# Optimization experiments

Measured on AMD Instinct MI355X. Metric: run time of the kernel, lower is better.

## Reference

```python
import jax, jax.numpy as jnp
import numpy as np

B, F, D, H = 16384, 10, 512, 8
DH = D // H
EPS = 1e-5


def setup_inputs() -> dict:
    key = jax.random.key(0)
    ks = jax.random.split(key, 12)
    s = 1.0 / np.sqrt(D)
    inp = {
        "x": jax.random.normal(ks[0], (B, F), dtype=jnp.float32),
        # per-feature Linear(1, D): weight (F, D), bias (F, D)
        "Wf": jax.random.normal(ks[1], (F, D), dtype=jnp.float32) * 1.0,
        "bf": jax.random.normal(ks[2], (F, D), dtype=jnp.float32) * 0.1,
        # MHA in/out projections (torch layout: out_features x in_features)
        "Wq": jax.random.normal(ks[3], (D, D), dtype=jnp.float32) * s,
        "Wk": jax.random.normal(ks[4], (D, D), dtype=jnp.float32) * s,
        "Wv": jax.random.normal(ks[5], (D, D), dtype=jnp.float32) * s,
        "bq": jax.random.normal(ks[6], (D,), dtype=jnp.float32) * 0.02,
        "bk": jax.random.normal(ks[7], (D,), dtype=jnp.float32) * 0.02,
        "bv": jax.random.normal(ks[8], (D,), dtype=jnp.float32) * 0.02,
        "Wo": jax.random.normal(ks[9], (D, D), dtype=jnp.float32) * s,
        "bo": jax.random.normal(ks[10], (D,), dtype=jnp.float32) * 0.02,
        "gamma": jnp.ones((D,), dtype=jnp.float32),
        "beta": jnp.zeros((D,), dtype=jnp.float32),
    }
    return inp


def reference(x, Wf, bf, Wq, Wk, Wv, bq, bk, bv, Wo, bo, gamma, beta):
    # Fused per-feature scalar Linear + ReLU: (B,F,1)*(F,D) + (F,D) -> (B,F,D)
    p = jax.nn.relu(x[:, :, None] * Wf[None] + bf[None])
    # Multi-head self-attention (q = k = v = p), torch Linear: y = x @ W.T + b
    def heads(t):  # (B,F,D) -> (B,H,F,DH)
        return t.reshape(B, F, H, DH).transpose(0, 2, 1, 3)
    q = heads(p @ Wq.T + bq)
    k = heads(p @ Wk.T + bk)
    v = heads(p @ Wv.T + bv)
    scores = jnp.einsum("bhqd,bhkd->bhqk", q, k) / jnp.sqrt(jnp.float32(DH))
    attn = jax.nn.softmax(scores, axis=-1)
    o = jnp.einsum("bhqk,bhkd->bhqd", attn, v)
    o = o.transpose(0, 2, 1, 3).reshape(B, F, D) @ Wo.T + bo
    # LayerNorm over last dim
    mu = jnp.mean(o, axis=-1, keepdims=True)
    var = jnp.mean(jnp.square(o - mu), axis=-1, keepdims=True)
    ln = (o - mu) * jax.lax.rsqrt(var + EPS) * gamma + beta
    # sum pool over the function/sequence axis
    return jnp.sum(ln, axis=1)  # (B, D)
```

## Files before the change

### kernel.cpp

```cpp
#include <hip/hip_runtime.h>
#include <stdint.h>


typedef __bf16 bf16;
typedef __bf16 bf16x8 __attribute__((ext_vector_type(8)));
typedef float f32x4 __attribute__((ext_vector_type(4)));

#define EPS 1e-5f

static constexpr size_t O_ELEMS   = (size_t)16384 * 10 * 512;
static constexpr size_t O_BYTES   = O_ELEMS * 2;
static constexpr size_t WQKV_ELEMS = (size_t)8 * 192 * 512;
static constexpr size_t WQKV_BYTES = WQKV_ELEMS * 2;

__device__ __forceinline__ void async_copy16(void* lds, const void* g) {
  __builtin_amdgcn_global_load_lds(
      (const __attribute__((address_space(1))) uint32_t*)g,
      (__attribute__((address_space(3))) uint32_t*)lds, 16, 0, 0);
}

__global__ __launch_bounds__(256) void pack_weights(
    const float* __restrict__ Wq, const float* __restrict__ Wk,
    const float* __restrict__ Wv, const float* __restrict__ Wo,
    bf16* __restrict__ wqkv, bf16* __restrict__ wob) {
  int idx = blockIdx.x * 256 + threadIdx.x;
#pragma unroll
  for (int u = 0; u < 4; ++u) {
    int i = idx + u * 262144;
    if (i < 786432) {
      int pr = i >> 9, k = i & 511;
      int h = pr / 192, w = pr - h * 192;
      int t = w >> 6, r = w & 63;
      const float* src = (t == 0) ? Wq : ((t == 1) ? Wk : Wv);
      wqkv[i] = (bf16)src[(h * 64 + r) * 512 + k];
    } else {
      int j = i - 786432;
      wob[j] = (bf16)Wo[j];
    }
  }
}

__global__ __launch_bounds__(256, 2) void kern_attn(
    const float* __restrict__ x, const float* __restrict__ Wf,
    const float* __restrict__ bfv, const bf16* __restrict__ wqkv,
    const float* __restrict__ bq, const float* __restrict__ bk,
    const float* __restrict__ bv, bf16* __restrict__ O) {
  __shared__ __align__(16) char sA[8 * 48 * 128];
  __shared__ __align__(16) char sU[24576];
  bf16* qkv = (bf16*)sU;
  float* sc = (float*)(sU + 19200);

  const int tid = threadIdx.x;
  const int wave = tid >> 6;
  const int lane = tid & 63;
  const int lm = lane & 15;
  const int lg = lane >> 4;
  const int b0 = blockIdx.x * 4;

#pragma unroll
  for (int it = 0; it < 12; ++it) {
    int c = tid + it * 256;
    int s = c / 384, rem = c - s * 384;
    int r = rem >> 3, kcp = rem & 7;
    int kc = kcp ^ (r & 7);
    int k = s * 64 + kc * 8;
    bf16x8 pv;
    if (r < 40) {
      int bl = r / 10, f = r - bl * 10;
      float xv = x[(b0 + bl) * 10 + f];
      const float* wf = Wf + f * 512 + k;
      const float* bp = bfv + f * 512 + k;
#pragma unroll
      for (int j = 0; j < 8; ++j) {
        float p = fmaxf(xv * wf[j] + bp[j], 0.f);
        pv[j] = (bf16)p;
      }
    } else {
#pragma unroll
      for (int j = 0; j < 8; ++j) pv[j] = (bf16)0.f;
    }
    *(bf16x8*)(sA + s * 6144 + r * 128 + kcp * 16) = pv;
  }

  const int lr = lane >> 3;
  const int kcp2 = lane & 7;
  const int kcg = kcp2 ^ lr;

  for (int h = 0; h < 8; ++h) {
    f32x4 acc[3][3];
#pragma unroll
    for (int i = 0; i < 3; ++i)
#pragma unroll
      for (int j = 0; j < 3; ++j) { f32x4 z = {0.f, 0.f, 0.f, 0.f}; acc[i][j] = z; }

    const bf16* wh = wqkv + (size_t)h * 192 * 512;

    for (int s = 0; s < 8; ++s) {
#pragma unroll
      for (int jb = 0; jb < 6; ++jb) {
        int rb = wave + 4 * jb;
        int rr = rb * 8 + lr;
        async_copy16(sU + rb * 1024, wh + (size_t)rr * 512 + s * 64 + kcg * 8);
      }
      __syncthreads();
#pragma unroll
      for (int kk = 0; kk < 2; ++kk) {
        int kcl = kk * 4 + lg;
        bf16x8 af[3], bfr[3];
#pragma unroll
        for (int mt = 0; mt < 3; ++mt) {
          int m = mt * 16 + lm;
          af[mt] = *(const bf16x8*)(sA + s * 6144 + m * 128 + ((kcl ^ (m & 7)) << 4));
        }
#pragma unroll
        for (int nt = 0; nt < 3; ++nt) {
          int n = wave * 48 + nt * 16 + lm;
          bfr[nt] = *(const bf16x8*)(sU + n * 128 + ((kcl ^ (n & 7)) << 4));
        }
#pragma unroll
        for (int mt = 0; mt < 3; ++mt)
#pragma unroll
          for (int nt = 0; nt < 3; ++nt)
            acc[mt][nt] = __builtin_amdgcn_mfma_f32_16x16x32_bf16(af[mt], bfr[nt], acc[mt][nt], 0, 0, 0);
      }
      __syncthreads();
    }

#pragma unroll
    for (int nt = 0; nt < 3; ++nt) {
      int col = wave * 48 + nt * 16 + lm;
      float bias;
      if (col < 64) bias = bq[h * 64 + col];
      else if (col < 128) bias = bk[h * 64 + col - 64];
      else bias = bv[h * 64 + col - 128];
#pragma unroll
      for (int mt = 0; mt < 3; ++mt)
#pragma unroll
        for (int r = 0; r < 4; ++r) {
          int row = mt * 16 + lg * 4 + r;
          if (row < 40) qkv[row * 200 + col] = (bf16)(acc[mt][nt][r] + bias);
        }
    }
    __syncthreads();

    {
      int b = wave;
#pragma unroll
      for (int pp = 0; pp < 2; ++pp) {
        int p = lane + pp * 64;
        if (p < 100) {
          int i = p / 10, j = p - i * 10;
          const bf16x8* qr = (const bf16x8*)(qkv + (b * 10 + i) * 200);
          const bf16x8* kr = (const bf16x8*)(qkv + (b * 10 + j) * 200 + 64);
          float d = 0.f;
#pragma unroll
          for (int c8 = 0; c8 < 8; ++c8) {
            bf16x8 qv = qr[c8], kv = kr[c8];
#pragma unroll
            for (int e = 0; e < 8; ++e) d += (float)qv[e] * (float)kv[e];
          }
          sc[(b * 10 + i) * 12 + j] = d * 0.125f;
        }
      }
    }
    __syncthreads();

    if (tid < 40) {
      float* row = sc + tid * 12;
      float m = row[0];
#pragma unroll
      for (int j = 1; j < 10; ++j) m = fmaxf(m, row[j]);
      float e[10], sum = 0.f;
#pragma unroll
      for (int j = 0; j < 10; ++j) { e[j] = __expf(row[j] - m); sum += e[j]; }
      float inv = 1.f / sum;
#pragma unroll
      for (int j = 0; j < 10; ++j) row[j] = e[j] * inv;
    }
    __syncthreads();

#pragma unroll
    for (int u = 0; u < 10; ++u) {
      int id = tid + u * 256;
      int b = id / 640, rem2 = id - b * 640;
      int i = rem2 >> 6, d = rem2 & 63;
      const float* ar = sc + (b * 10 + i) * 12;
      float o = 0.f;
#pragma unroll
      for (int j = 0; j < 10; ++j)
        o += ar[j] * (float)qkv[(b * 10 + j) * 200 + 128 + d];
      O[((size_t)(b0 + b) * 10 + i) * 512 + h * 64 + d] = (bf16)o;
    }
    __syncthreads();
  }
}

__global__ __launch_bounds__(256, 2) void kern_out(
    const bf16* __restrict__ O, const bf16* __restrict__ wob,
    const float* __restrict__ bo, const float* __restrict__ gamma,
    const float* __restrict__ beta, float* __restrict__ out) {
  __shared__ __align__(16) char sAB[71680];
  __shared__ float partial[48][4][2];
  __shared__ float stats[48][2];
  char* As = sAB;
  char* Bs = sAB + 6144;
  bf16* lnb = (bf16*)sAB;

  const int tid = threadIdx.x;
  const int wave = tid >> 6, lane = tid & 63;
  const int lm = lane & 15, lg = lane >> 4;
  const int m0 = blockIdx.x * 40;

  f32x4 acc[3][8];
#pragma unroll
  for (int i = 0; i < 3; ++i)
#pragma unroll
    for (int j = 0; j < 8; ++j) { f32x4 z = {0.f, 0.f, 0.f, 0.f}; acc[i][j] = z; }

  const int lr = lane >> 3;
  const int kcp2 = lane & 7;
  const int kcg = kcp2 ^ lr;

  for (int s = 0; s < 8; ++s) {
    {
      int rr = wave * 8 + lr;
      int rm = min(rr, 39);
      async_copy16(As + wave * 1024, O + (size_t)(m0 + rm) * 512 + s * 64 + kcg * 8);
      if (wave < 2) {
        int rr2 = (4 + wave) * 8 + lr;
        int rm2 = min(rr2, 39);
        async_copy16(As + (4 + wave) * 1024, O + (size_t)(m0 + rm2) * 512 + s * 64 + kcg * 8);
      }
    }
#pragma unroll
    for (int jb = 0; jb < 16; ++jb) {
      int rb = wave + 4 * jb;
      int n = rb * 8 + lr;
      async_copy16(Bs + rb * 1024, wob + (size_t)n * 512 + s * 64 + kcg * 8);
    }
    __syncthreads();
#pragma unroll
    for (int kk = 0; kk < 2; ++kk) {
      int kcl = kk * 4 + lg;
      bf16x8 af[3], bfr[8];
#pragma unroll
      for (int mt = 0; mt < 3; ++mt) {
        int m = mt * 16 + lm;
        af[mt] = *(const bf16x8*)(As + m * 128 + ((kcl ^ (m & 7)) << 4));
      }
#pragma unroll
      for (int nt = 0; nt < 8; ++nt) {
        int n = wave * 128 + nt * 16 + lm;
        bfr[nt] = *(const bf16x8*)(Bs + n * 128 + ((kcl ^ (n & 7)) << 4));
      }
#pragma unroll
      for (int mt = 0; mt < 3; ++mt)
#pragma unroll
        for (int nt = 0; nt < 8; ++nt)
          acc[mt][nt] = __builtin_amdgcn_mfma_f32_16x16x32_bf16(af[mt], bfr[nt], acc[mt][nt], 0, 0, 0);
    }
    __syncthreads();
  }

#pragma unroll
  for (int nt = 0; nt < 8; ++nt) {
    int col = wave * 128 + nt * 16 + lm;
    float bb = bo[col];
#pragma unroll
    for (int mt = 0; mt < 3; ++mt)
#pragma unroll
      for (int r = 0; r < 4; ++r) acc[mt][nt][r] += bb;
  }

#pragma unroll
  for (int mt = 0; mt < 3; ++mt)
#pragma unroll
    for (int r = 0; r < 4; ++r) {
      float s1 = 0.f, s2 = 0.f;
#pragma unroll
      for (int nt = 0; nt < 8; ++nt) { float v = acc[mt][nt][r]; s1 += v; s2 += v * v; }
#pragma unroll
      for (int off = 1; off < 16; off <<= 1) {
        s1 += __shfl_xor(s1, off);
        s2 += __shfl_xor(s2, off);
      }
      if (lm == 0) {
        int row = mt * 16 + lg * 4 + r;
        partial[row][wave][0] = s1;
        partial[row][wave][1] = s2;
      }
    }
  __syncthreads();
  if (tid < 48) {
    float s1 = partial[tid][0][0] + partial[tid][1][0] + partial[tid][2][0] + partial[tid][3][0];
    float s2 = partial[tid][0][1] + partial[tid][1][1] + partial[tid][2][1] + partial[tid][3][1];
    float mu = s1 * (1.f / 512.f);
    float var = s2 * (1.f / 512.f) - mu * mu;
    stats[tid][0] = mu;
    stats[tid][1] = rsqrtf(var + EPS);
  }
  __syncthreads();
#pragma unroll
  for (int mt = 0; mt < 3; ++mt)
#pragma unroll
    for (int r = 0; r < 4; ++r) {
      int row = mt * 16 + lg * 4 + r;
      float mu = stats[row][0], rr = stats[row][1];
#pragma unroll
      for (int nt = 0; nt < 8; ++nt) {
        int col = wave * 128 + nt * 16 + lm;
        lnb[row * 520 + col] = (bf16)((acc[mt][nt][r] - mu) * rr);
      }
    }
  __syncthreads();
#pragma unroll
  for (int u = 0; u < 8; ++u) {
    int id = tid + u * 256;
    int b = id >> 9, n = id & 511;
    float ssum = 0.f;
#pragma unroll
    for (int f = 0; f < 10; ++f) ssum += (float)lnb[(b * 10 + f) * 520 + n];
    out[(size_t)(blockIdx.x * 4 + b) * 512 + n] = gamma[n] * ssum + 10.f * beta[n];
  }
}

extern "C" void kernel_launch(void* const* d_in, const int* in_sizes, int n_in,
                              void* d_out, int out_size, void* d_ws, size_t ws_size,
                              hipStream_t stream) {
  const float* x     = (const float*)d_in[0];
  const float* Wf    = (const float*)d_in[1];
  const float* bfv   = (const float*)d_in[2];
  const float* Wq    = (const float*)d_in[3];
  const float* Wk    = (const float*)d_in[4];
  const float* Wv    = (const float*)d_in[5];
  const float* bq    = (const float*)d_in[6];
  const float* bk    = (const float*)d_in[7];
  const float* bv    = (const float*)d_in[8];
  const float* Wo    = (const float*)d_in[9];
  const float* bo    = (const float*)d_in[10];
  const float* gamma = (const float*)d_in[11];
  const float* beta  = (const float*)d_in[12];
  float* out = (float*)d_out;

  char* ws = (char*)d_ws;
  bf16* O    = (bf16*)ws;
  bf16* wqkv = (bf16*)(ws + O_BYTES);
  bf16* wob  = (bf16*)(ws + O_BYTES + WQKV_BYTES);

  pack_weights<<<1024, 256, 0, stream>>>(Wq, Wk, Wv, Wo, wqkv, wob);
  kern_attn<<<4096, 256, 0, stream>>>(x, Wf, bfv, wqkv, bq, bk, bv, O);
  kern_out<<<4096, 256, 0, stream>>>(O, wob, bo, gamma, beta, out);
}
```

Measured before the change: 842.9 us.

## Give each wave its own heads with double-buffered weights and MFMA attention

The attention kernel now assigns whole heads to individual waves, two heads per wave, instead of splitting each head's QKV columns across the four waves. Each wave streams its head's weight slices into a private double-buffered LDS region using async loads and vmcnt waits, so block-wide barriers are gone from the main loop. Scores and the attention-times-V product are computed with MFMA over a block-diagonal 40x40 tile, with masked softmax done through shuffles and normalization deferred to the output. The trade-off is much more LDS per block and more registers (launch bounds drop to one block per CU), plus wasted MFMA work on the masked off-diagonal entries.

Result: slower. 910.1 us (+8.0%).

```diff
diff --git a/kernel.cpp b/kernel.cpp
--- a/kernel.cpp
+++ b/kernel.cpp
@@ -10,14 +10,15 @@
 
 static constexpr size_t O_ELEMS   = (size_t)16384 * 10 * 512;
 static constexpr size_t O_BYTES   = O_ELEMS * 2;
-static constexpr size_t WQKV_ELEMS = (size_t)8 * 192 * 512;
-static constexpr size_t WQKV_BYTES = WQKV_ELEMS * 2;
+static constexpr size_t WQKV_BYTES = (size_t)8 * 192 * 512 * 2;
 
 __device__ __forceinline__ void async_copy16(void* lds, const void* g) {
   __builtin_amdgcn_global_load_lds(
       (const __attribute__((address_space(1))) uint32_t*)g,
       (__attribute__((address_space(3))) uint32_t*)lds, 16, 0, 0);
 }
+__device__ __forceinline__ void wait_vmcnt_0()  { __builtin_amdgcn_s_waitcnt(0x0F70); }
+__device__ __forceinline__ void wait_vmcnt_12() { __builtin_amdgcn_s_waitcnt(0x0F70 | 12); }
 
 __global__ __launch_bounds__(256) void pack_weights(
     const float* __restrict__ Wq, const float* __restrict__ Wk,
@@ -40,15 +41,13 @@
   }
 }
 
-__global__ __launch_bounds__(256, 2) void kern_attn(
+__global__ __launch_bounds__(256, 1) void kern_attn(
     const float* __restrict__ x, const float* __restrict__ Wf,
     const float* __restrict__ bfv, const bf16* __restrict__ wqkv,
     const float* __restrict__ bq, const float* __restrict__ bk,
     const float* __restrict__ bv, bf16* __restrict__ O) {
-  __shared__ __align__(16) char sA[8 * 48 * 128];
-  __shared__ __align__(16) char sU[24576];
-  bf16* qkv = (bf16*)sU;
-  float* sc = (float*)(sU + 19200);
+  __shared__ __align__(16) char sA[49152];
+  __shared__ __align__(16) char sW[4][24576];
 
   const int tid = threadIdx.x;
   const int wave = tid >> 6;
@@ -71,127 +70,191 @@
       const float* wf = Wf + f * 512 + k;
       const float* bp = bfv + f * 512 + k;
 #pragma unroll
-      for (int j = 0; j < 8; ++j) {
-        float p = fmaxf(xv * wf[j] + bp[j], 0.f);
-        pv[j] = (bf16)p;
-      }
+      for (int j = 0; j < 8; ++j) pv[j] = (bf16)fmaxf(xv * wf[j] + bp[j], 0.f);
     } else {
 #pragma unroll
       for (int j = 0; j < 8; ++j) pv[j] = (bf16)0.f;
     }
     *(bf16x8*)(sA + s * 6144 + r * 128 + kcp * 16) = pv;
   }
-
-  const int lr = lane >> 3;
-  const int kcp2 = lane & 7;
-  const int kcg = kcp2 ^ lr;
-
-  for (int h = 0; h < 8; ++h) {
-    f32x4 acc[3][3];
+  __syncthreads();
+
+  char* reg  = sW[wave];
+  char* qbuf = reg;
+  char* kbuf = reg + 6912;
+  char* vtb  = reg + 13824;
+
+  const int rlo = lane >> 2, cpn = lane & 3;
+  const int bswiz = ((lg ^ (lm & 3) ^ ((lm >> 2) & 3)) << 4);
+
+  for (int hh = 0; hh < 2; ++hh) {
+    const int h = wave + hh * 4;
+    const bf16* wh = wqkv + (size_t)h * 192 * 512;
+
+    float bias[12];
+#pragma unroll
+    for (int nt = 0; nt < 12; ++nt) {
+      int col = nt * 16 + lm;
+      const float* bp = (col < 64) ? (bq + h * 64 + col)
+                       : (col < 128) ? (bk + h * 64 + col - 64)
+                                     : (bv + h * 64 + col - 128);
+      bias[nt] = *bp;
+    }
+
+    f32x4 acc[3][12];
 #pragma unroll
     for (int i = 0; i < 3; ++i)
 #pragma unroll
-      for (int j = 0; j < 3; ++j) { f32x4 z = {0.f, 0.f, 0.f, 0.f}; acc[i][j] = z; }
-
-    const bf16* wh = wqkv + (size_t)h * 192 * 512;
-
-    for (int s = 0; s < 8; ++s) {
-#pragma unroll
-      for (int jb = 0; jb < 6; ++jb) {
-        int rb = wave + 4 * jb;
-        int rr = rb * 8 + lr;
-        async_copy16(sU + rb * 1024, wh + (size_t)rr * 512 + s * 64 + kcg * 8);
-      }
-      __syncthreads();
-#pragma unroll
-      for (int kk = 0; kk < 2; ++kk) {
-        int kcl = kk * 4 + lg;
-        bf16x8 af[3], bfr[3];
-#pragma unroll
-        for (int mt = 0; mt < 3; ++mt) {
-          int m = mt * 16 + lm;
-          af[mt] = *(const bf16x8*)(sA + s * 6144 + m * 128 + ((kcl ^ (m & 7)) << 4));
+      for (int j = 0; j < 12; ++j) { f32x4 z = {0.f, 0.f, 0.f, 0.f}; acc[i][j] = z; }
+
+#pragma unroll
+    for (int j = 0; j < 12; ++j) {
+      int r = j * 16 + rlo;
+      int cg = cpn ^ (r & 3) ^ ((r >> 2) & 3);
+      async_copy16(reg + j * 1024, wh + (size_t)r * 512 + cg * 8);
+    }
+
+    for (int s = 0; s < 16; ++s) {
+      if (s < 15) {
+        char* dst = reg + ((s + 1) & 1) * 12288;
+        int ks = (s + 1) * 32;
+#pragma unroll
+        for (int j = 0; j < 12; ++j) {
+          int r = j * 16 + rlo;
+          int cg = cpn ^ (r & 3) ^ ((r >> 2) & 3);
+          async_copy16(dst + j * 1024, wh + (size_t)r * 512 + ks + cg * 8);
         }
-#pragma unroll
-        for (int nt = 0; nt < 3; ++nt) {
-          int n = wave * 48 + nt * 16 + lm;
-          bfr[nt] = *(const bf16x8*)(sU + n * 128 + ((kcl ^ (n & 7)) << 4));
-        }
+        wait_vmcnt_12();
+      } else {
+        wait_vmcnt_0();
+      }
+      const char* buf = reg + (s & 1) * 12288;
+      const char* sAs = sA + (s >> 1) * 6144;
+      int kc = ((s & 1) << 2) | lg;
+      bf16x8 af[3];
+#pragma unroll
+      for (int mt = 0; mt < 3; ++mt) {
+        int m = mt * 16 + lm;
+        af[mt] = *(const bf16x8*)(sAs + m * 128 + ((kc ^ (m & 7)) << 4));
+      }
+#pragma unroll
+      for (int nt = 0; nt < 12; ++nt) {
+        bf16x8 bfr = *(const bf16x8*)(buf + (nt * 16 + lm) * 64 + bswiz);
 #pragma unroll
         for (int mt = 0; mt < 3; ++mt)
-#pragma unroll
-          for (int nt = 0; nt < 3; ++nt)
-            acc[mt][nt] = __builtin_amdgcn_mfma_f32_16x16x32_bf16(af[mt], bfr[nt], acc[mt][nt], 0, 0, 0);
-      }
-      __syncthreads();
-    }
-
-#pragma unroll
-    for (int nt = 0; nt < 3; ++nt) {
-      int col = wave * 48 + nt * 16 + lm;
-      float bias;
-      if (col < 64) bias = bq[h * 64 + col];
-      else if (col < 128) bias = bk[h * 64 + col - 64];
-      else bias = bv[h * 64 + col - 128];
+          acc[mt][nt] = __builtin_amdgcn_mfma_f32_16x16x32_bf16(af[mt], bfr, acc[mt][nt], 0, 0, 0);
+      }
+    }
+
+    {
+      f32x4 z4 = {0.f, 0.f, 0.f, 0.f};
+      *(f32x4*)(vtb + lane * 144 + 80)  = z4;
+      *(f32x4*)(vtb + lane * 144 + 96)  = z4;
+      *(f32x4*)(vtb + lane * 144 + 112) = z4;
+    }
+#pragma unroll
+    for (int nt = 0; nt < 12; ++nt) {
+      int col = nt * 16 + lm;
 #pragma unroll
       for (int mt = 0; mt < 3; ++mt)
 #pragma unroll
         for (int r = 0; r < 4; ++r) {
           int row = mt * 16 + lg * 4 + r;
-          if (row < 40) qkv[row * 200 + col] = (bf16)(acc[mt][nt][r] + bias);
+          if (row < 40) {
+            float v = acc[mt][nt][r] + bias[nt];
+            if (col < 64)       *(bf16*)(qbuf + row * 144 + col * 2) = (bf16)(v * 0.125f);
+            else if (col < 128) *(bf16*)(kbuf + row * 144 + (col - 64) * 2) = (bf16)v;
+            else                *(bf16*)(vtb + (col - 128) * 144 + row * 2) = (bf16)v;
+          }
         }
     }
-    __syncthreads();
-
-    {
-      int b = wave;
-#pragma unroll
-      for (int pp = 0; pp < 2; ++pp) {
-        int p = lane + pp * 64;
-        if (p < 100) {
-          int i = p / 10, j = p - i * 10;
-          const bf16x8* qr = (const bf16x8*)(qkv + (b * 10 + i) * 200);
-          const bf16x8* kr = (const bf16x8*)(qkv + (b * 10 + j) * 200 + 64);
-          float d = 0.f;
-#pragma unroll
-          for (int c8 = 0; c8 < 8; ++c8) {
-            bf16x8 qv = qr[c8], kv = kr[c8];
-#pragma unroll
-            for (int e = 0; e < 8; ++e) d += (float)qv[e] * (float)kv[e];
+
+    f32x4 accS[3][3];
+#pragma unroll
+    for (int i = 0; i < 3; ++i)
+#pragma unroll
+      for (int j = 0; j < 3; ++j) { f32x4 z = {0.f, 0.f, 0.f, 0.f}; accS[i][j] = z; }
+#pragma unroll
+    for (int kk = 0; kk < 2; ++kk) {
+      bf16x8 aq[3], bk8[3];
+#pragma unroll
+      for (int mt = 0; mt < 3; ++mt)
+        aq[mt] = *(const bf16x8*)(qbuf + (mt * 16 + lm) * 144 + kk * 64 + lg * 16);
+#pragma unroll
+      for (int nt = 0; nt < 3; ++nt)
+        bk8[nt] = *(const bf16x8*)(kbuf + (nt * 16 + lm) * 144 + kk * 64 + lg * 16);
+#pragma unroll
+      for (int mt = 0; mt < 3; ++mt)
+#pragma unroll
+        for (int nt = 0; nt < 3; ++nt)
+          accS[mt][nt] = __builtin_amdgcn_mfma_f32_16x16x32_bf16(aq[mt], bk8[nt], accS[mt][nt], 0, 0, 0);
+    }
+
+    float inv_r[3][4];
+#pragma unroll
+    for (int mt = 0; mt < 3; ++mt)
+#pragma unroll
+      for (int r = 0; r < 4; ++r) {
+        int row = mt * 16 + lg * 4 + r;
+        int c0 = (row / 10) * 10;
+        float vv[3]; bool val[3];
+#pragma unroll
+        for (int nt = 0; nt < 3; ++nt) {
+          int col = nt * 16 + lm;
+          vv[nt] = accS[mt][nt][r];
+          val[nt] = ((unsigned)(col - c0)) < 10u;
+        }
+        float m = -3.0e38f;
+#pragma unroll
+        for (int nt = 0; nt < 3; ++nt) m = val[nt] ? fmaxf(m, vv[nt]) : m;
+#pragma unroll
+        for (int off = 1; off < 16; off <<= 1) m = fmaxf(m, __shfl_xor(m, off));
+        float e[3], ssum = 0.f;
+#pragma unroll
+        for (int nt = 0; nt < 3; ++nt) { e[nt] = val[nt] ? __expf(vv[nt] - m) : 0.f; ssum += e[nt]; }
+#pragma unroll
+        for (int off = 1; off < 16; off <<= 1) ssum += __shfl_xor(ssum, off);
+        inv_r[mt][r] = 1.0f / ssum;
+#pragma unroll
+        for (int nt = 0; nt < 3; ++nt)
+          *(bf16*)(qbuf + row * 144 + (nt * 16 + lm) * 2) = (bf16)e[nt];
+        *(bf16*)(qbuf + row * 144 + (48 + lm) * 2) = (bf16)0.f;
+      }
+
+    f32x4 accO[3][4];
+#pragma unroll
+    for (int i = 0; i < 3; ++i)
+#pragma unroll
+      for (int j = 0; j < 4; ++j) { f32x4 z = {0.f, 0.f, 0.f, 0.f}; accO[i][j] = z; }
+#pragma unroll
+    for (int kk = 0; kk < 2; ++kk) {
+      bf16x8 aa[3], bv8[4];
+#pragma unroll
+      for (int mt = 0; mt < 3; ++mt)
+        aa[mt] = *(const bf16x8*)(qbuf + (mt * 16 + lm) * 144 + kk * 64 + lg * 16);
+#pragma unroll
+      for (int nt = 0; nt < 4; ++nt)
+        bv8[nt] = *(const bf16x8*)(vtb + (nt * 16 + lm) * 144 + kk * 64 + lg * 16);
+#pragma unroll
+      for (int mt = 0; mt < 3; ++mt)
+#pragma unroll
+        for (int nt = 0; nt < 4; ++nt)
+          accO[mt][nt] = __builtin_amdgcn_mfma_f32_16x16x32_bf16(aa[mt], bv8[nt], accO[mt][nt], 0, 0, 0);
+    }
+#pragma unroll
+    for (int mt = 0; mt < 3; ++mt)
+#pragma unroll
+      for (int r = 0; r < 4; ++r) {
+        int row = mt * 16 + lg * 4 + r;
+        if (row < 40) {
+          float scl = inv_r[mt][r];
+#pragma unroll
+          for (int nt = 0; nt < 4; ++nt) {
+            int d = nt * 16 + lm;
+            O[(size_t)(b0 * 10 + row) * 512 + h * 64 + d] = (bf16)(accO[mt][nt][r] * scl);
           }
-          sc[(b * 10 + i) * 12 + j] = d * 0.125f;
         }
       }
-    }
-    __syncthreads();
-
-    if (tid < 40) {
-      float* row = sc + tid * 12;
-      float m = row[0];
-#pragma unroll
-      for (int j = 1; j < 10; ++j) m = fmaxf(m, row[j]);
-      float e[10], sum = 0.f;
-#pragma unroll
-      for (int j = 0; j < 10; ++j) { e[j] = __expf(row[j] - m); sum += e[j]; }
-      float inv = 1.f / sum;
-#pragma unroll
-      for (int j = 0; j < 10; ++j) row[j] = e[j] * inv;
-    }
-    __syncthreads();
-
-#pragma unroll
-    for (int u = 0; u < 10; ++u) {
-      int id = tid + u * 256;
-      int b = id / 640, rem2 = id - b * 640;
-      int i = rem2 >> 6, d = rem2 & 63;
-      const float* ar = sc + (b * 10 + i) * 12;
-      float o = 0.f;
-#pragma unroll
-      for (int j = 0; j < 10; ++j)
-        o += ar[j] * (float)qkv[(b * 10 + j) * 200 + 128 + d];
-      O[((size_t)(b0 + b) * 10 + i) * 512 + h * 64 + d] = (bf16)o;
-    }
-    __syncthreads();
   }
 }
 
```

## Double-buffer per-wave weight tiles with vmcnt waits instead of block barriers

Applied to the files above, without the earlier changes.

Both GEMM kernels now give each wave a private LDS region for its slice of the weight matrix. A two-stage double buffer is driven by s_waitcnt vmcnt counts, which replaces the per-k-step __syncthreads pairs. In kern_out the A operand (attention output O) is loaded straight from global into registers with a prefetch, instead of being staged through LDS. In kern_attn the weights for the next head are prefetched during the softmax/PV phase. This should hide global-load latency and remove barrier stalls, but it relies on precise vmcnt accounting, and the direct-to-register A loads are unswizzled and uncoalesced.

New measurement: 1.288 ms. +52.8%, slower.

```diff
diff --git a/kernel.cpp b/kernel.cpp
--- a/kernel.cpp
+++ b/kernel.cpp
@@ -10,14 +10,14 @@
 
 static constexpr size_t O_ELEMS   = (size_t)16384 * 10 * 512;
 static constexpr size_t O_BYTES   = O_ELEMS * 2;
-static constexpr size_t WQKV_ELEMS = (size_t)8 * 192 * 512;
-static constexpr size_t WQKV_BYTES = WQKV_ELEMS * 2;
+static constexpr size_t WQKV_BYTES = (size_t)8 * 192 * 512 * 2;
 
 __device__ __forceinline__ void async_copy16(void* lds, const void* g) {
   __builtin_amdgcn_global_load_lds(
       (const __attribute__((address_space(1))) uint32_t*)g,
       (__attribute__((address_space(3))) uint32_t*)lds, 16, 0, 0);
 }
+#define WAIT_VM(n) __builtin_amdgcn_s_waitcnt(0x0F70 | (n))
 
 __global__ __launch_bounds__(256) void pack_weights(
     const float* __restrict__ Wq, const float* __restrict__ Wk,
@@ -45,17 +45,25 @@
     const float* __restrict__ bfv, const bf16* __restrict__ wqkv,
     const float* __restrict__ bq, const float* __restrict__ bk,
     const float* __restrict__ bv, bf16* __restrict__ O) {
-  __shared__ __align__(16) char sA[8 * 48 * 128];
-  __shared__ __align__(16) char sU[24576];
-  bf16* qkv = (bf16*)sU;
-  float* sc = (float*)(sU + 19200);
+  __shared__ __align__(16) char sA[49152];
+  __shared__ __align__(16) char sB[24576];
+  bf16* qkv = (bf16*)sB;
+  float* sc = (float*)(sB + 19200);
 
   const int tid = threadIdx.x;
-  const int wave = tid >> 6;
-  const int lane = tid & 63;
-  const int lm = lane & 15;
-  const int lg = lane >> 4;
+  const int wave = tid >> 6, lane = tid & 63;
+  const int lm = lane & 15, lg = lane >> 4;
   const int b0 = blockIdx.x * 4;
+
+  char* myB = sB + wave * 6144;
+  const int srow = lane & 15;
+  const int schunk = lane >> 4;
+  const bf16* wbase = wqkv + (size_t)(48 * wave + srow) * 512 + schunk * 8;
+
+#pragma unroll
+  for (int c = 0; c < 3; ++c) async_copy16(myB + c * 1024, wbase + (size_t)c * 8192);
+#pragma unroll
+  for (int c = 0; c < 3; ++c) async_copy16(myB + 3072 + c * 1024, wbase + (size_t)c * 8192 + 32);
 
 #pragma unroll
   for (int it = 0; it < 12; ++it) {
@@ -71,20 +79,14 @@
       const float* wf = Wf + f * 512 + k;
       const float* bp = bfv + f * 512 + k;
 #pragma unroll
-      for (int j = 0; j < 8; ++j) {
-        float p = fmaxf(xv * wf[j] + bp[j], 0.f);
-        pv[j] = (bf16)p;
-      }
+      for (int j = 0; j < 8; ++j) pv[j] = (bf16)fmaxf(xv * wf[j] + bp[j], 0.f);
     } else {
 #pragma unroll
       for (int j = 0; j < 8; ++j) pv[j] = (bf16)0.f;
     }
     *(bf16x8*)(sA + s * 6144 + r * 128 + kcp * 16) = pv;
   }
-
-  const int lr = lane >> 3;
-  const int kcp2 = lane & 7;
-  const int kcg = kcp2 ^ lr;
+  __syncthreads();
 
   for (int h = 0; h < 8; ++h) {
     f32x4 acc[3][3];
@@ -93,38 +95,34 @@
 #pragma unroll
       for (int j = 0; j < 3; ++j) { f32x4 z = {0.f, 0.f, 0.f, 0.f}; acc[i][j] = z; }
 
-    const bf16* wh = wqkv + (size_t)h * 192 * 512;
-
-    for (int s = 0; s < 8; ++s) {
-#pragma unroll
-      for (int jb = 0; jb < 6; ++jb) {
-        int rb = wave + 4 * jb;
-        int rr = rb * 8 + lr;
-        async_copy16(sU + rb * 1024, wh + (size_t)rr * 512 + s * 64 + kcg * 8);
-      }
-      __syncthreads();
-#pragma unroll
-      for (int kk = 0; kk < 2; ++kk) {
-        int kcl = kk * 4 + lg;
-        bf16x8 af[3], bfr[3];
-#pragma unroll
-        for (int mt = 0; mt < 3; ++mt) {
-          int m = mt * 16 + lm;
-          af[mt] = *(const bf16x8*)(sA + s * 6144 + m * 128 + ((kcl ^ (m & 7)) << 4));
-        }
-#pragma unroll
-        for (int nt = 0; nt < 3; ++nt) {
-          int n = wave * 48 + nt * 16 + lm;
-          bfr[nt] = *(const bf16x8*)(sU + n * 128 + ((kcl ^ (n & 7)) << 4));
-        }
-#pragma unroll
-        for (int mt = 0; mt < 3; ++mt)
-#pragma unroll
-          for (int nt = 0; nt < 3; ++nt)
-            acc[mt][nt] = __builtin_amdgcn_mfma_f32_16x16x32_bf16(af[mt], bfr[nt], acc[mt][nt], 0, 0, 0);
-      }
-      __syncthreads();
-    }
+#pragma unroll
+    for (int s = 0; s < 16; ++s) {
+      if (s < 15) WAIT_VM(3); else WAIT_VM(0);
+      const char* buf = myB + (s & 1) * 3072;
+      const char* sAs = sA + (s >> 1) * 6144;
+      const int kc = (s & 1) * 4 + lg;
+      bf16x8 af[3], bfr[3];
+#pragma unroll
+      for (int mt = 0; mt < 3; ++mt) {
+        int m = mt * 16 + lm;
+        af[mt] = *(const bf16x8*)(sAs + m * 128 + ((kc ^ (m & 7)) << 4));
+      }
+#pragma unroll
+      for (int nt = 0; nt < 3; ++nt)
+        bfr[nt] = *(const bf16x8*)(buf + nt * 1024 + lg * 256 + lm * 16);
+#pragma unroll
+      for (int mt = 0; mt < 3; ++mt)
+#pragma unroll
+        for (int nt = 0; nt < 3; ++nt)
+          acc[mt][nt] = __builtin_amdgcn_mfma_f32_16x16x32_bf16(af[mt], bfr[nt], acc[mt][nt], 0, 0, 0);
+      if (s < 14) {
+#pragma unroll
+        for (int c = 0; c < 3; ++c)
+          async_copy16(myB + (s & 1) * 3072 + c * 1024,
+                       wbase + (size_t)h * 98304 + (size_t)c * 8192 + (s + 2) * 32);
+      }
+    }
+    __syncthreads();
 
 #pragma unroll
     for (int nt = 0; nt < 3; ++nt) {
@@ -192,24 +190,44 @@
       O[((size_t)(b0 + b) * 10 + i) * 512 + h * 64 + d] = (bf16)o;
     }
     __syncthreads();
+
+    if (h < 7) {
+#pragma unroll
+      for (int c = 0; c < 3; ++c)
+        async_copy16(myB + c * 1024, wbase + (size_t)(h + 1) * 98304 + (size_t)c * 8192);
+#pragma unroll
+      for (int c = 0; c < 3; ++c)
+        async_copy16(myB + 3072 + c * 1024,
+                     wbase + (size_t)(h + 1) * 98304 + (size_t)c * 8192 + 32);
+    }
   }
 }
 
 __global__ __launch_bounds__(256, 2) void kern_out(
-    const bf16* __restrict__ O, const bf16* __restrict__ wob,
+    const bf16* __restrict__ Oin, const bf16* __restrict__ wob,
     const float* __restrict__ bo, const float* __restrict__ gamma,
     const float* __restrict__ beta, float* __restrict__ out) {
-  __shared__ __align__(16) char sAB[71680];
-  __shared__ float partial[48][4][2];
-  __shared__ float stats[48][2];
-  char* As = sAB;
-  char* Bs = sAB + 6144;
-  bf16* lnb = (bf16*)sAB;
+  __shared__ __align__(16) char smem[67456];
+  char* B2 = smem;
+  float* partial = (float*)(smem + 65536);
+  float* stats = (float*)(smem + 65536 + 1536);
+  bf16* lnb = (bf16*)smem;
 
   const int tid = threadIdx.x;
   const int wave = tid >> 6, lane = tid & 63;
   const int lm = lane & 15, lg = lane >> 4;
   const int m0 = blockIdx.x * 40;
+  const int srow = lane & 15, schunk = lane >> 4;
+
+  char* myB = B2 + wave * 16384;
+  const bf16* wb = wob + (size_t)(128 * wave + srow) * 512 + schunk * 8;
+
+  const bf16* arow[3];
+#pragma unroll
+  for (int mt = 0; mt < 3; ++mt) {
+    int r = mt * 16 + lm; if (r > 39) r = 39;
+    arow[mt] = Oin + (size_t)(m0 + r) * 512 + lg * 8;
+  }
 
   f32x4 acc[3][8];
 #pragma unroll
@@ -217,49 +235,41 @@
 #pragma unroll
     for (int j = 0; j < 8; ++j) { f32x4 z = {0.f, 0.f, 0.f, 0.f}; acc[i][j] = z; }
 
-  const int lr = lane >> 3;
-  const int kcp2 = lane & 7;
-  const int kcg = kcp2 ^ lr;
-
-  for (int s = 0; s < 8; ++s) {
-    {
-      int rr = wave * 8 + lr;
-      int rm = min(rr, 39);
-      async_copy16(As + wave * 1024, O + (size_t)(m0 + rm) * 512 + s * 64 + kcg * 8);
-      if (wave < 2) {
-        int rr2 = (4 + wave) * 8 + lr;
-        int rm2 = min(rr2, 39);
-        async_copy16(As + (4 + wave) * 1024, O + (size_t)(m0 + rm2) * 512 + s * 64 + kcg * 8);
-      }
-    }
-#pragma unroll
-    for (int jb = 0; jb < 16; ++jb) {
-      int rb = wave + 4 * jb;
-      int n = rb * 8 + lr;
-      async_copy16(Bs + rb * 1024, wob + (size_t)n * 512 + s * 64 + kcg * 8);
-    }
-    __syncthreads();
-#pragma unroll
-    for (int kk = 0; kk < 2; ++kk) {
-      int kcl = kk * 4 + lg;
-      bf16x8 af[3], bfr[8];
-#pragma unroll
-      for (int mt = 0; mt < 3; ++mt) {
-        int m = mt * 16 + lm;
-        af[mt] = *(const bf16x8*)(As + m * 128 + ((kcl ^ (m & 7)) << 4));
-      }
-#pragma unroll
-      for (int nt = 0; nt < 8; ++nt) {
-        int n = wave * 128 + nt * 16 + lm;
-        bfr[nt] = *(const bf16x8*)(Bs + n * 128 + ((kcl ^ (n & 7)) << 4));
-      }
+#pragma unroll
+  for (int c = 0; c < 8; ++c)
+    async_copy16(myB + c * 1024, wb + (size_t)c * 8192);
+#pragma unroll
+  for (int c = 0; c < 8; ++c)
+    async_copy16(myB + 8192 + c * 1024, wb + (size_t)c * 8192 + 32);
+  bf16x8 afp[2][3];
+#pragma unroll
+  for (int mt = 0; mt < 3; ++mt) afp[0][mt] = *(const bf16x8*)(arow[mt]);
+#pragma unroll
+  for (int mt = 0; mt < 3; ++mt) afp[1][mt] = *(const bf16x8*)(arow[mt] + 32);
+
+#pragma unroll
+  for (int s = 0; s < 16; ++s) {
+    if (s == 0) WAIT_VM(3);
+    else if (s < 15) WAIT_VM(11);
+    else WAIT_VM(0);
+    const char* buf = myB + (s & 1) * 8192;
+    bf16x8 bfr[8];
+#pragma unroll
+    for (int nt = 0; nt < 8; ++nt)
+      bfr[nt] = *(const bf16x8*)(buf + nt * 1024 + lg * 256 + lm * 16);
+#pragma unroll
+    for (int mt = 0; mt < 3; ++mt)
+#pragma unroll
+      for (int nt = 0; nt < 8; ++nt)
+        acc[mt][nt] = __builtin_amdgcn_mfma_f32_16x16x32_bf16(afp[s & 1][mt], bfr[nt], acc[mt][nt], 0, 0, 0);
+    if (s < 14) {
 #pragma unroll
       for (int mt = 0; mt < 3; ++mt)
-#pragma unroll
-        for (int nt = 0; nt < 8; ++nt)
-          acc[mt][nt] = __builtin_amdgcn_mfma_f32_16x16x32_bf16(af[mt], bfr[nt], acc[mt][nt], 0, 0, 0);
-    }
-    __syncthreads();
+        afp[s & 1][mt] = *(const bf16x8*)(arow[mt] + (s + 2) * 32);
+#pragma unroll
+      for (int c = 0; c < 8; ++c)
+        async_copy16(myB + (s & 1) * 8192 + c * 1024, wb + (size_t)c * 8192 + (s + 2) * 32);
+    }
   }
 
 #pragma unroll
@@ -286,18 +296,18 @@
       }
       if (lm == 0) {
         int row = mt * 16 + lg * 4 + r;
-        partial[row][wave][0] = s1;
-        partial[row][wave][1] = s2;
+        partial[row * 8 + wave * 2 + 0] = s1;
+        partial[row * 8 + wave * 2 + 1] = s2;
       }
     }
   __syncthreads();
   if (tid < 48) {
-    float s1 = partial[tid][0][0] + partial[tid][1][0] + partial[tid][2][0] + partial[tid][3][0];
-    float s2 = partial[tid][0][1] + partial[tid][1][1] + partial[tid][2][1] + partial[tid][3][1];
+    float s1 = partial[tid * 8 + 0] + partial[tid * 8 + 2] + partial[tid * 8 + 4] + partial[tid * 8 + 6];
+    float s2 = partial[tid * 8 + 1] + partial[tid * 8 + 3] + partial[tid * 8 + 5] + partial[tid * 8 + 7];
     float mu = s1 * (1.f / 512.f);
     float var = s2 * (1.f / 512.f) - mu * mu;
-    stats[tid][0] = mu;
-    stats[tid][1] = rsqrtf(var + EPS);
+    stats[tid * 2 + 0] = mu;
+    stats[tid * 2 + 1] = rsqrtf(var + EPS);
   }
   __syncthreads();
 #pragma unroll
@@ -305,7 +315,7 @@
 #pragma unroll
     for (int r = 0; r < 4; ++r) {
       int row = mt * 16 + lg * 4 + r;
-      float mu = stats[row][0], rr = stats[row][1];
+      float mu = stats[row * 2 + 0], rr = stats[row * 2 + 1];
 #pragma unroll
       for (int nt = 0; nt < 8; ++nt) {
         int col = wave * 128 + nt * 16 + lm;
```

## Compute attention scores with MFMA and per-wave softmax via shuffles

Applied to the files above, without the earlier changes.

Stores Q (pre-scaled), K and V for each batch row in a per-wave swizzled LDS tile, then computes the 10x10 score matrix with two bf16 MFMA instructions per wave instead of scalar dot products. Softmax is done in registers with 16-lane xor shuffles, and the AV product is done per wave without block-wide barriers between the score, softmax and AV stages. This removes two __syncthreads per head and the scalar dot-product loops. The cost is wasted MFMA lanes on padded rows and columns, and an added rounding step because Q is scaled before the bf16 cast.

After: 887.0 us. +5.2%, slower.

```diff
diff --git a/kernel.cpp b/kernel.cpp
--- a/kernel.cpp
+++ b/kernel.cpp
@@ -10,14 +10,14 @@
 
 static constexpr size_t O_ELEMS   = (size_t)16384 * 10 * 512;
 static constexpr size_t O_BYTES   = O_ELEMS * 2;
-static constexpr size_t WQKV_ELEMS = (size_t)8 * 192 * 512;
-static constexpr size_t WQKV_BYTES = WQKV_ELEMS * 2;
+static constexpr size_t WQKV_BYTES = (size_t)8 * 192 * 512 * 2;
 
 __device__ __forceinline__ void async_copy16(void* lds, const void* g) {
   __builtin_amdgcn_global_load_lds(
       (const __attribute__((address_space(1))) uint32_t*)g,
       (__attribute__((address_space(3))) uint32_t*)lds, 16, 0, 0);
 }
+__device__ __forceinline__ void wait_lgkm0() { __builtin_amdgcn_s_waitcnt(0xC07F); }
 
 __global__ __launch_bounds__(256) void pack_weights(
     const float* __restrict__ Wq, const float* __restrict__ Wk,
@@ -45,16 +45,12 @@
     const float* __restrict__ bfv, const bf16* __restrict__ wqkv,
     const float* __restrict__ bq, const float* __restrict__ bk,
     const float* __restrict__ bv, bf16* __restrict__ O) {
-  __shared__ __align__(16) char sA[8 * 48 * 128];
-  __shared__ __align__(16) char sU[24576];
-  bf16* qkv = (bf16*)sU;
-  float* sc = (float*)(sU + 19200);
+  __shared__ __align__(16) char sA[49152];
+  __shared__ __align__(16) char sB[24576];
 
   const int tid = threadIdx.x;
-  const int wave = tid >> 6;
-  const int lane = tid & 63;
-  const int lm = lane & 15;
-  const int lg = lane >> 4;
+  const int wave = tid >> 6, lane = tid & 63;
+  const int lm = lane & 15, lg = lane >> 4;
   const int b0 = blockIdx.x * 4;
 
 #pragma unroll
@@ -71,20 +67,19 @@
       const float* wf = Wf + f * 512 + k;
       const float* bp = bfv + f * 512 + k;
 #pragma unroll
-      for (int j = 0; j < 8; ++j) {
-        float p = fmaxf(xv * wf[j] + bp[j], 0.f);
-        pv[j] = (bf16)p;
-      }
+      for (int j = 0; j < 8; ++j) pv[j] = (bf16)fmaxf(xv * wf[j] + bp[j], 0.f);
     } else {
 #pragma unroll
       for (int j = 0; j < 8; ++j) pv[j] = (bf16)0.f;
     }
     *(bf16x8*)(sA + s * 6144 + r * 128 + kcp * 16) = pv;
   }
+  __syncthreads();
 
   const int lr = lane >> 3;
   const int kcp2 = lane & 7;
   const int kcg = kcp2 ^ lr;
+  char* wbase = sB + wave * 6144;
 
   for (int h = 0; h < 8; ++h) {
     f32x4 acc[3][3];
@@ -93,14 +88,14 @@
 #pragma unroll
       for (int j = 0; j < 3; ++j) { f32x4 z = {0.f, 0.f, 0.f, 0.f}; acc[i][j] = z; }
 
-    const bf16* wh = wqkv + (size_t)h * 192 * 512;
+    const bf16* wh = wqkv + (size_t)h * 98304;
 
     for (int s = 0; s < 8; ++s) {
 #pragma unroll
       for (int jb = 0; jb < 6; ++jb) {
         int rb = wave + 4 * jb;
         int rr = rb * 8 + lr;
-        async_copy16(sU + rb * 1024, wh + (size_t)rr * 512 + s * 64 + kcg * 8);
+        async_copy16(sB + rb * 1024, wh + (size_t)rr * 512 + s * 64 + kcg * 8);
       }
       __syncthreads();
 #pragma unroll
@@ -115,7 +110,7 @@
 #pragma unroll
         for (int nt = 0; nt < 3; ++nt) {
           int n = wave * 48 + nt * 16 + lm;
-          bfr[nt] = *(const bf16x8*)(sU + n * 128 + ((kcl ^ (n & 7)) << 4));
+          bfr[nt] = *(const bf16x8*)(sB + n * 128 + ((kcl ^ (n & 7)) << 4));
         }
 #pragma unroll
         for (int mt = 0; mt < 3; ++mt)
@@ -138,58 +133,60 @@
 #pragma unroll
         for (int r = 0; r < 4; ++r) {
           int row = mt * 16 + lg * 4 + r;
-          if (row < 40) qkv[row * 200 + col] = (bf16)(acc[mt][nt][r] + bias);
+          if (row < 40) {
+            int b = row / 10, i = row - b * 10;
+            char* tb = sB + b * 6144;
+            float v = acc[mt][nt][r] + bias;
+            if (col < 64) {
+              int c = col, oct = c >> 3;
+              *(bf16*)(tb + i * 128 + ((oct ^ (i & 7)) << 4) + (c & 7) * 2) = (bf16)(v * 0.125f);
+            } else if (col < 128) {
+              int c = col - 64, oct = c >> 3;
+              *(bf16*)(tb + 2048 + i * 128 + ((oct ^ (i & 7)) << 4) + (c & 7) * 2) = (bf16)v;
+            } else {
+              int c = col - 128;
+              *(bf16*)(tb + 4096 + i * 128 + c * 2) = (bf16)v;
+            }
+          }
         }
     }
     __syncthreads();
 
-    {
-      int b = wave;
-#pragma unroll
-      for (int pp = 0; pp < 2; ++pp) {
-        int p = lane + pp * 64;
-        if (p < 100) {
-          int i = p / 10, j = p - i * 10;
-          const bf16x8* qr = (const bf16x8*)(qkv + (b * 10 + i) * 200);
-          const bf16x8* kr = (const bf16x8*)(qkv + (b * 10 + j) * 200 + 64);
-          float d = 0.f;
-#pragma unroll
-          for (int c8 = 0; c8 < 8; ++c8) {
-            bf16x8 qv = qr[c8], kv = kr[c8];
-#pragma unroll
-            for (int e = 0; e < 8; ++e) d += (float)qv[e] * (float)kv[e];
-          }
-          sc[(b * 10 + i) * 12 + j] = d * 0.125f;
-        }
-      }
-    }
-    __syncthreads();
-
-    if (tid < 40) {
-      float* row = sc + tid * 12;
-      float m = row[0];
-#pragma unroll
-      for (int j = 1; j < 10; ++j) m = fmaxf(m, row[j]);
-      float e[10], sum = 0.f;
-#pragma unroll
-      for (int j = 0; j < 10; ++j) { e[j] = __expf(row[j] - m); sum += e[j]; }
-      float inv = 1.f / sum;
-#pragma unroll
-      for (int j = 0; j < 10; ++j) row[j] = e[j] * inv;
-    }
-    __syncthreads();
-
-#pragma unroll
-    for (int u = 0; u < 10; ++u) {
-      int id = tid + u * 256;
-      int b = id / 640, rem2 = id - b * 640;
-      int i = rem2 >> 6, d = rem2 & 63;
-      const float* ar = sc + (b * 10 + i) * 12;
+    f32x4 s4 = {0.f, 0.f, 0.f, 0.f};
+#pragma unroll
+    for (int kk = 0; kk < 2; ++kk) {
+      int oct = kk * 4 + lg;
+      bf16x8 qf = *(const bf16x8*)(wbase + lm * 128 + ((oct ^ (lm & 7)) << 4));
+      bf16x8 kf = *(const bf16x8*)(wbase + 2048 + lm * 128 + ((oct ^ (lm & 7)) << 4));
+      s4 = __builtin_amdgcn_mfma_f32_16x16x32_bf16(qf, kf, s4, 0, 0, 0);
+    }
+    float* aL = (float*)(wbase + 5376);
+#pragma unroll
+    for (int r = 0; r < 4; ++r) {
+      int i = lg * 4 + r;
+      float val = s4[r];
+      float m = (lm < 10) ? val : -3.0e38f;
+#pragma unroll
+      for (int off = 1; off < 16; off <<= 1) m = fmaxf(m, __shfl_xor(m, off));
+      float e = (lm < 10) ? __expf(val - m) : 0.f;
+      float sum = e;
+#pragma unroll
+      for (int off = 1; off < 16; off <<= 1) sum += __shfl_xor(sum, off);
+      if (i < 10 && lm < 10) aL[i * 10 + lm] = e / sum;
+    }
+    wait_lgkm0();
+
+    float vj[10];
+#pragma unroll
+    for (int j = 0; j < 10; ++j)
+      vj[j] = (float)*(const bf16*)(wbase + 4096 + j * 128 + lane * 2);
+    const size_t obase = ((size_t)(b0 + wave) * 10) * 512 + (size_t)h * 64 + lane;
+#pragma unroll
+    for (int i = 0; i < 10; ++i) {
       float o = 0.f;
 #pragma unroll
-      for (int j = 0; j < 10; ++j)
-        o += ar[j] * (float)qkv[(b * 10 + j) * 200 + 128 + d];
-      O[((size_t)(b0 + b) * 10 + i) * 512 + h * 64 + d] = (bf16)o;
+      for (int j = 0; j < 10; ++j) o += aL[i * 10 + j] * vj[j];
+      O[obase + (size_t)i * 512] = (bf16)o;
     }
     __syncthreads();
   }
```
